# Optimization experiments

Measured on AMD Instinct MI355X. Metric: run time of the kernel, lower is better.

## Reference

```python
import math
import jax, jax.numpy as jnp
import numpy as np

CAPACITY_FACTOR = 1.25
TOP_K = 2
LN_EPS = 1e-5


def setup_inputs() -> dict:
    key = jax.random.key(0)
    ks = jax.random.split(key, 4)
    B, S, D, F, E = 8, 4096, 256, 512, 8
    x = jax.random.normal(ks[0], (B, S, D), dtype=jnp.float32)
    Wr = jax.random.normal(ks[1], (D, E), dtype=jnp.float32) / np.sqrt(D)
    br = jnp.zeros((E,), jnp.float32)
    W1 = jax.random.normal(ks[2], (E, D, F), dtype=jnp.float32) / np.sqrt(D)
    b1 = jnp.zeros((E, F), jnp.float32)
    W2 = jax.random.normal(ks[3], (E, F, D), dtype=jnp.float32) / np.sqrt(F)
    b2 = jnp.zeros((E, D), jnp.float32)
    gamma = jnp.ones((D,), jnp.float32)
    beta = jnp.zeros((D,), jnp.float32)
    return {"x": x, "Wr": Wr, "br": br, "W1": W1, "b1": b1,
            "W2": W2, "b2": b2, "gamma": gamma, "beta": beta}


def _layer_norm(x, gamma, beta):
    mu = jnp.mean(x, axis=-1, keepdims=True)
    var = jnp.var(x, axis=-1, keepdims=True)
    return (x - mu) * jax.lax.rsqrt(var + LN_EPS) * gamma + beta


def reference(x, Wr, br, W1, b1, W2, b2, gamma, beta):
    B, S, D = x.shape
    E = Wr.shape[1]
    N = B * S
    K = TOP_K

    # --- Router: per-sequence softmax routing weights [B, E] ---
    logits = jnp.mean(x, axis=1) @ Wr + br              # [B, E]
    routing_weights = jax.nn.softmax(logits, axis=-1)   # [B, E]

    # --- Capacity constraints (SparseMoELayer._apply_capacity_constraints) ---
    capacity = float(math.ceil(N * CAPACITY_FACTOR / E))
    expected_loads = routing_weights.sum(axis=0) * (N / B)          # [E]
    scale = jnp.where(expected_loads > capacity,
                      capacity / expected_loads, 1.0)               # [E]
    routing_weights = jax.nn.softmax(routing_weights * scale, axis=-1)

    # --- Expand to tokens and take top-k, renormalize with softmax ---
    rw_tok = jnp.broadcast_to(routing_weights[:, None, :], (B, S, E)).reshape(N, E)
    top_w, top_i = jax.lax.top_k(rw_tok, K)             # [N, K]
    top_w = jax.nn.softmax(top_w, axis=-1)

    # --- Expert FFNs (dense compute over all experts, sparse combine) ---
    xf = x.reshape(N, D)
    h = jax.nn.gelu(jnp.einsum('nd,edf->enf', xf, W1) + b1[:, None, :],
                    approximate=False)                  # [E, N, F]
    y = jnp.einsum('enf,efd->end', h, W2) + b2[:, None, :]  # [E, N, D]

    # dense combine weights [N, E] via scatter-add of top-k weights
    w_dense = jnp.zeros((N, E), x.dtype).at[jnp.arange(N)[:, None], top_i].add(top_w)
    out = jnp.einsum('ne,end->nd', w_dense, y).reshape(B, S, D)

    # residual + layer norm
    out = _layer_norm(out + x, gamma, beta)
    return out
```

## Files before the change

kernel.cpp:

```cpp
#include <hip/hip_runtime.h>
#include <math.h>


#define B_ 8
#define S_ 4096
#define D_ 256
#define F_ 512
#define E_ 8

typedef short bf16x8 __attribute__((ext_vector_type(8)));
typedef float f32x4 __attribute__((ext_vector_type(4)));

static __device__ __forceinline__ unsigned short f2bf(float f) {
    union { float f; unsigned int i; } v; v.f = f;
    unsigned int x = v.i;
    return (unsigned short)((x + 0x7fffu + ((x >> 16) & 1u)) >> 16);
}

static __device__ __forceinline__ void bar_lds() {
    asm volatile("s_waitcnt lgkmcnt(0)" ::: "memory");
    __builtin_amdgcn_s_barrier();
}

static __device__ __forceinline__ float gelu_f(float v) {
    float x = fabsf(v) * 0.70710678118654752f;
    float t = __builtin_amdgcn_rcpf(1.0f + 0.3275911f * x);
    float p = t * (0.254829592f +
              t * (-0.284496736f +
              t * (1.421413741f +
              t * (-1.453152027f +
              t * 1.061405429f))));
    float er = 1.0f - p * __expf(-x * x);
    er = __builtin_copysignf(er, v);
    return 0.5f * v * (1.0f + er);
}

__global__ void k_prep(const float* __restrict__ x,
                       double* __restrict__ partial,
                       const float* __restrict__ W1,
                       const float* __restrict__ W2,
                       unsigned short* __restrict__ W1T,
                       unsigned short* __restrict__ W2T) {
    int bid = blockIdx.x;
    if (bid < 512) {
        int b = bid >> 6;
        int c = bid & 63;
        int d = threadIdx.x;
        const float* p = x + ((size_t)(b * S_ + c * 64) * D_ + d);
        double acc = 0.0;
        #pragma unroll 8
        for (int i = 0; i < 64; ++i) acc += (double)p[(size_t)i * D_];
        partial[(size_t)bid * D_ + d] = acc;
        return;
    }
    __shared__ float tile[32][33];
    const float* src;
    unsigned short* dst;
    int R, C, cb, rb;
    if (bid < 1536) {
        int b2 = bid - 512;
        int e = b2 >> 7, rem = b2 & 127;
        int by = rem >> 4, bx = rem & 15;
        R = 256; C = 512;
        src = W1 + (size_t)e * R * C;
        dst = W1T + (size_t)e * R * C;
        cb = bx * 32; rb = by * 32;
    } else {
        int b2 = bid - 1536;
        int e = b2 >> 7, rem = b2 & 127;
        int by = rem >> 3, bx = rem & 7;
        R = 512; C = 256;
        src = W2 + (size_t)e * R * C;
        dst = W2T + (size_t)e * R * C;
        cb = bx * 32; rb = by * 32;
    }
    int tx = threadIdx.x & 31, ty = threadIdx.x >> 5;
    #pragma unroll
    for (int k = 0; k < 4; ++k)
        tile[ty + 8 * k][tx] = src[(size_t)(rb + ty + 8 * k) * C + cb + tx];
    __syncthreads();
    #pragma unroll
    for (int k = 0; k < 4; ++k)
        dst[(size_t)(cb + ty + 8 * k) * R + rb + tx] = f2bf(tile[tx][ty + 8 * k]);
}

__global__ void k_finish(const double* __restrict__ partial,
                         const float* __restrict__ Wr,
                         const float* __restrict__ br,
                         float* __restrict__ route) {
    __shared__ double xs[8][256];
    __shared__ double lg[64];
    __shared__ double rw[8][8];
    int t = threadIdx.x;
    #pragma unroll
    for (int pp = 0; pp < 2; ++pp) {
        int p = pp * 1024 + t;
        int bb = p >> 8, d = p & 255;
        double acc = 0.0;
        #pragma unroll 8
        for (int c = 0; c < 64; ++c)
            acc += partial[(size_t)(bb * 64 + c) * D_ + d];
        xs[bb][d] = acc;
    }
    __syncthreads();
    if (t < 64) {
        int b = t >> 3, e = t & 7;
        double acc = 0.0;
        for (int d = 0; d < D_; ++d)
            acc += (xs[b][d] * (1.0 / (double)S_)) * (double)Wr[d * E_ + e];
        lg[t] = acc + (double)br[e];
    }
    __syncthreads();
    if (t < 8) {
        int bb = t;
        double m = -1e300;
        for (int ee = 0; ee < 8; ++ee) m = fmax(m, lg[bb * 8 + ee]);
        double s = 0.0;
        double p[8];
        for (int ee = 0; ee < 8; ++ee) { p[ee] = exp(lg[bb * 8 + ee] - m); s += p[ee]; }
        for (int ee = 0; ee < 8; ++ee) rw[bb][ee] = p[ee] / s;
    }
    __syncthreads();
    if (t < 8) {
        int bb = t;
        const double capacity = 5120.0;
        double scale[8];
        for (int ee = 0; ee < 8; ++ee) {
            double load = 0.0;
            for (int b2 = 0; b2 < 8; ++b2) load += rw[b2][ee];
            load *= 4096.0;
            scale[ee] = load > capacity ? capacity / load : 1.0;
        }
        double v[8];
        double m = -1e300;
        for (int ee = 0; ee < 8; ++ee) { v[ee] = rw[bb][ee] * scale[ee]; m = fmax(m, v[ee]); }
        double s = 0.0;
        for (int ee = 0; ee < 8; ++ee) { v[ee] = exp(v[ee] - m); s += v[ee]; }
        for (int ee = 0; ee < 8; ++ee) v[ee] /= s;
        int i1 = 0;
        for (int ee = 1; ee < 8; ++ee) if (v[ee] > v[i1]) i1 = ee;
        int i2 = (i1 == 0) ? 1 : 0;
        for (int ee = 0; ee < 8; ++ee) { if (ee == i1) continue; if (v[ee] > v[i2]) i2 = ee; }
        double d21 = v[i2] - v[i1];
        double ed = exp(d21);
        double w1 = 1.0 / (1.0 + ed);
        double w2 = ed * w1;
        route[bb * 4 + 0] = (float)i1;
        route[bb * 4 + 1] = (float)i2;
        route[bb * 4 + 2] = (float)w1;
        route[bb * 4 + 3] = (float)w2;
    }
}

__launch_bounds__(512, 4)
__global__ void k_moe_m(const float* __restrict__ xf,
                        const unsigned short* __restrict__ W1T,
                        const unsigned short* __restrict__ W2T,
                        const float* __restrict__ b1,
                        const float* __restrict__ b2,
                        const float* __restrict__ gamma,
                        const float* __restrict__ beta,
                        const float* __restrict__ route,
                        float* __restrict__ out) {
    __shared__ __align__(16) unsigned short Xsb[64][264];
    __shared__ __align__(16) unsigned short Hsb[2][64][136];
    __shared__ float gbuf[256], bbuf[256];
    __shared__ __align__(16) float rred[64][20];

    const int t = threadIdx.x;
    const int wv = t >> 6;
    const int lane = t & 63;
    const int g = lane >> 4;
    const int c = lane & 15;
    const int b = blockIdx.x & 7;
    const int m0 = (blockIdx.x >> 3) * 64;

    if (t < 256) { gbuf[t] = gamma[t]; bbuf[t] = beta[t]; }

    {
        int row = t >> 3;
        int col0 = (t & 7) * 32;
        const float* src = xf + ((size_t)(b * S_ + m0 + row) * D_ + col0);
        #pragma unroll
        for (int jg = 0; jg < 4; ++jg) {
            float4 a0 = *(const float4*)(src + jg * 8);
            float4 a1 = *(const float4*)(src + jg * 8 + 4);
            float vv[8] = { a0.x, a0.y, a0.z, a0.w, a1.x, a1.y, a1.z, a1.w };
            union { unsigned short u[8]; uint4 q; } o;
            #pragma unroll
            for (int j = 0; j < 8; ++j) o.u[j] = f2bf(vv[j]);
            *(uint4*)&Xsb[row][col0 + jg * 8] = o.q;
        }
    }

    const int e0i = (int)route[b * 4 + 0];
    const int e1i = (int)route[b * 4 + 1];
    const float rw0 = route[b * 4 + 2];
    const float rw1 = route[b * 4 + 3];
    const int eidx[2] = { e0i, e1i };
    const float wgt[2] = { rw0, rw1 };

    f32x4 Yacc[4][2];
    #pragma unroll
    for (int i = 0; i < 4; ++i)
        #pragma unroll
        for (int j = 0; j < 2; ++j)
            #pragma unroll
            for (int r = 0; r < 4; ++r) Yacc[i][j][r] = 0.f;

    bar_lds();

    int pb = 0;
    for (int sl = 0; sl < 2; ++sl) {
        const int e = eidx[sl];
        const float w = wgt[sl];
        for (int fb = 0; fb < 4; ++fb) {
            const unsigned short* w1p =
                W1T + ((size_t)(e * F_ + fb * 128 + wv * 16 + c)) * D_ + g * 8;
            bf16x8 w1f[8];
            #pragma unroll
            for (int kc = 0; kc < 8; ++kc)
                w1f[kc] = *(const bf16x8*)(w1p + kc * 32);
            const unsigned short* w2p =
                W2T + ((size_t)(e * D_ + wv * 32 + c)) * F_ + fb * 128 + g * 8;
            bf16x8 w2f[4][2];
            #pragma unroll
            for (int kc = 0; kc < 4; ++kc)
                #pragma unroll
                for (int nt = 0; nt < 2; ++nt)
                    w2f[kc][nt] = *(const bf16x8*)(w2p + (size_t)(nt * 16) * F_ + kc * 32);
            asm volatile("" : "+v"(w1f[0]), "+v"(w1f[1]), "+v"(w1f[2]), "+v"(w1f[3]),
                              "+v"(w1f[4]), "+v"(w1f[5]), "+v"(w1f[6]), "+v"(w1f[7]));

            f32x4 Hacc[4];
            #pragma unroll
            for (int i = 0; i < 4; ++i)
                #pragma unroll
                for (int r = 0; r < 4; ++r) Hacc[i][r] = 0.f;
            #pragma unroll
            for (int kc = 0; kc < 8; ++kc) {
                #pragma unroll
                for (int mt = 0; mt < 4; ++mt) {
                    bf16x8 a = *(const bf16x8*)&Xsb[mt * 16 + c][kc * 32 + g * 8];
                    Hacc[mt] = __builtin_amdgcn_mfma_f32_16x16x32_bf16(a, w1f[kc], Hacc[mt], 0, 0, 0);
                }
            }

            {
                float bias1 = b1[e * F_ + fb * 128 + wv * 16 + c];
                #pragma unroll
                for (int mt = 0; mt < 4; ++mt)
                    #pragma unroll
                    for (int r = 0; r < 4; ++r) {
                        int row = mt * 16 + g * 4 + r;
                        float v = Hacc[mt][r] + bias1;
                        Hsb[pb][row][wv * 16 + c] = f2bf(w * gelu_f(v));
                    }
            }
            asm volatile("" : "+v"(w2f[0][0]), "+v"(w2f[0][1]), "+v"(w2f[1][0]), "+v"(w2f[1][1]),
                              "+v"(w2f[2][0]), "+v"(w2f[2][1]), "+v"(w2f[3][0]), "+v"(w2f[3][1]));
            bar_lds();

            #pragma unroll
            for (int kc = 0; kc < 4; ++kc) {
                #pragma unroll
                for (int mt = 0; mt < 4; ++mt) {
                    bf16x8 a = *(const bf16x8*)&Hsb[pb][mt * 16 + c][kc * 32 + g * 8];
                    #pragma unroll
                    for (int nt = 0; nt < 2; ++nt)
                        Yacc[mt][nt] = __builtin_amdgcn_mfma_f32_16x16x32_bf16(a, w2f[kc][nt], Yacc[mt][nt], 0, 0, 0);
                }
            }
            pb ^= 1;
        }
    }

    float bias2[2];
    #pragma unroll
    for (int nt = 0; nt < 2; ++nt) {
        int d = wv * 32 + nt * 16 + c;
        bias2[nt] = rw0 * b2[e0i * D_ + d] + rw1 * b2[e1i * D_ + d];
    }
    #pragma unroll
    for (int mt = 0; mt < 4; ++mt)
        #pragma unroll
        for (int r = 0; r < 4; ++r) {
            int row = mt * 16 + g * 4 + r;
            const float* xr = xf + (size_t)(b * S_ + m0 + row) * D_;
            float s = 0.f, sq = 0.f;
            #pragma unroll
            for (int nt = 0; nt < 2; ++nt) {
                int d = wv * 32 + nt * 16 + c;
                float v = Yacc[mt][nt][r] + bias2[nt] + xr[d];
                Yacc[mt][nt][r] = v;
                s += v; sq += v * v;
            }
            s += __shfl_xor(s, 1); sq += __shfl_xor(sq, 1);
            s += __shfl_xor(s, 2); sq += __shfl_xor(sq, 2);
            s += __shfl_xor(s, 4); sq += __shfl_xor(sq, 4);
            s += __shfl_xor(s, 8); sq += __shfl_xor(sq, 8);
            if (c == 0) { rred[row][wv * 2] = s; rred[row][wv * 2 + 1] = sq; }
        }
    bar_lds();
    #pragma unroll
    for (int mt = 0; mt < 4; ++mt)
        #pragma unroll
        for (int r = 0; r < 4; ++r) {
            int row = mt * 16 + g * 4 + r;
            float4 p0 = *(const float4*)&rred[row][0];
            float4 p1 = *(const float4*)&rred[row][4];
            float4 p2 = *(const float4*)&rred[row][8];
            float4 p3 = *(const float4*)&rred[row][12];
            float s  = ((p0.x + p1.x) + (p2.x + p3.x)) + ((p0.z + p1.z) + (p2.z + p3.z));
            float sq = ((p0.y + p1.y) + (p2.y + p3.y)) + ((p0.w + p1.w) + (p2.w + p3.w));
            float mu = s * (1.0f / 256.0f);
            float var = sq * (1.0f / 256.0f) - mu * mu;
            float rstd = rsqrtf(var + 1e-5f);
            float* op = out + (size_t)(b * S_ + m0 + row) * D_;
            #pragma unroll
            for (int nt = 0; nt < 2; ++nt) {
                int d = wv * 32 + nt * 16 + c;
                op[d] = (Yacc[mt][nt][r] - mu) * rstd * gbuf[d] + bbuf[d];
            }
        }
}

extern "C" void kernel_launch(void* const* d_in, const int* in_sizes, int n_in,
                              void* d_out, int out_size, void* d_ws, size_t ws_size,
                              hipStream_t stream) {
    const float* x     = (const float*)d_in[0];
    const float* Wr    = (const float*)d_in[1];
    const float* br    = (const float*)d_in[2];
    const float* W1    = (const float*)d_in[3];
    const float* b1    = (const float*)d_in[4];
    const float* W2    = (const float*)d_in[5];
    const float* b2    = (const float*)d_in[6];
    const float* gamma = (const float*)d_in[7];
    const float* beta  = (const float*)d_in[8];
    float* out = (float*)d_out;

    char* ws = (char*)d_ws;
    double* partial = (double*)ws;
    float* route  = (float*)(ws + 1064960);
    unsigned short* W1T = (unsigned short*)(ws + 1081344);
    unsigned short* W2T = (unsigned short*)(ws + 3178496);

    hipLaunchKernelGGL(k_prep, dim3(2560), dim3(256), 0, stream,
                       x, partial, W1, W2, W1T, W2T);
    hipLaunchKernelGGL(k_finish, dim3(1), dim3(1024), 0, stream,
                       partial, Wr, br, route);
    hipLaunchKernelGGL(k_moe_m, dim3(512), dim3(512), 0, stream,
                       x, W1T, W2T, b1, b2, gamma, beta, route, out);
}
```

Measured before the change: 222.1 us.

## Prefetch next W1 fragment across flattened expert loop and use packed bf16 converts

Flattens the two-level expert/F-block loop into a single eight-iteration loop and issues the W1 fragment loads for the next iteration before the barrier and second GEMM, so global weight latency overlaps with compute. It also replaces the software bf16 rounding with the hardware v_cvt_pk_bf16_f32 instruction for the X staging and the GELU output. The prefetch keeps an extra set of fragment registers live, which may raise register pressure, and the final iteration wastefully reloads the first block.

```diff
diff --git a/kernel.cpp b/kernel.cpp
--- a/kernel.cpp
+++ b/kernel.cpp
@@ -15,6 +15,12 @@
     union { float f; unsigned int i; } v; v.f = f;
     unsigned int x = v.i;
     return (unsigned short)((x + 0x7fffu + ((x >> 16) & 1u)) >> 16);
+}
+
+static __device__ __forceinline__ unsigned int cvt_pk_bf16(float s0, float s1) {
+    unsigned int r;
+    asm("v_cvt_pk_bf16_f32 %0, %1, %2" : "=v"(r) : "v"(s0), "v"(s1));
+    return r;
 }
 
 static __device__ __forceinline__ void bar_lds() {
@@ -177,6 +183,11 @@
 
     if (t < 256) { gbuf[t] = gamma[t]; bbuf[t] = beta[t]; }
 
+    const int e0i = (int)route[b * 4 + 0];
+    const int e1i = (int)route[b * 4 + 1];
+    const float rw0 = route[b * 4 + 2];
+    const float rw1 = route[b * 4 + 3];
+
     {
         int row = t >> 3;
         int col0 = (t & 7) * 32;
@@ -185,21 +196,15 @@
         for (int jg = 0; jg < 4; ++jg) {
             float4 a0 = *(const float4*)(src + jg * 8);
             float4 a1 = *(const float4*)(src + jg * 8 + 4);
-            float vv[8] = { a0.x, a0.y, a0.z, a0.w, a1.x, a1.y, a1.z, a1.w };
-            union { unsigned short u[8]; uint4 q; } o;
-            #pragma unroll
-            for (int j = 0; j < 8; ++j) o.u[j] = f2bf(vv[j]);
+            union { unsigned int pk[4]; uint4 q; } o;
+            o.pk[0] = cvt_pk_bf16(a0.x, a0.y);
+            o.pk[1] = cvt_pk_bf16(a0.z, a0.w);
+            o.pk[2] = cvt_pk_bf16(a1.x, a1.y);
+            o.pk[3] = cvt_pk_bf16(a1.z, a1.w);
             *(uint4*)&Xsb[row][col0 + jg * 8] = o.q;
         }
     }
 
-    const int e0i = (int)route[b * 4 + 0];
-    const int e1i = (int)route[b * 4 + 1];
-    const float rw0 = route[b * 4 + 2];
-    const float rw1 = route[b * 4 + 3];
-    const int eidx[2] = { e0i, e1i };
-    const float wgt[2] = { rw0, rw1 };
-
     f32x4 Yacc[4][2];
     #pragma unroll
     for (int i = 0; i < 4; ++i)
@@ -208,71 +213,91 @@
             #pragma unroll
             for (int r = 0; r < 4; ++r) Yacc[i][j][r] = 0.f;
 
+    bf16x8 w1f[8];
+    {
+        const unsigned short* w1p0 =
+            W1T + ((size_t)(e0i * F_ + wv * 16 + c)) * D_ + g * 8;
+        #pragma unroll
+        for (int kc = 0; kc < 8; ++kc)
+            w1f[kc] = *(const bf16x8*)(w1p0 + kc * 32);
+    }
+
     bar_lds();
 
     int pb = 0;
-    for (int sl = 0; sl < 2; ++sl) {
-        const int e = eidx[sl];
-        const float w = wgt[sl];
-        for (int fb = 0; fb < 4; ++fb) {
-            const unsigned short* w1p =
-                W1T + ((size_t)(e * F_ + fb * 128 + wv * 16 + c)) * D_ + g * 8;
-            bf16x8 w1f[8];
+    for (int it = 0; it < 8; ++it) {
+        const int sl = it >> 2;
+        const int fb = it & 3;
+        const int e = sl ? e1i : e0i;
+        const float w = sl ? rw1 : rw0;
+
+        const unsigned short* w2p =
+            W2T + ((size_t)(e * D_ + wv * 32 + c)) * F_ + fb * 128 + g * 8;
+        bf16x8 w2f[4][2];
+        #pragma unroll
+        for (int kc = 0; kc < 4; ++kc)
+            #pragma unroll
+            for (int nt = 0; nt < 2; ++nt)
+                w2f[kc][nt] = *(const bf16x8*)(w2p + (size_t)(nt * 16) * F_ + kc * 32);
+
+        float bias1 = b1[e * F_ + fb * 128 + wv * 16 + c];
+
+        f32x4 Hacc[4];
+        #pragma unroll
+        for (int i = 0; i < 4; ++i)
+            #pragma unroll
+            for (int r = 0; r < 4; ++r) Hacc[i][r] = 0.f;
+        #pragma unroll
+        for (int kc = 0; kc < 8; ++kc) {
+            #pragma unroll
+            for (int mt = 0; mt < 4; ++mt) {
+                bf16x8 a = *(const bf16x8*)&Xsb[mt * 16 + c][kc * 32 + g * 8];
+                Hacc[mt] = __builtin_amdgcn_mfma_f32_16x16x32_bf16(a, w1f[kc], Hacc[mt], 0, 0, 0);
+            }
+        }
+
+        {
+            const int col = wv * 16 + c;
+            #pragma unroll
+            for (int mt = 0; mt < 4; ++mt) {
+                float h0 = w * gelu_f(Hacc[mt][0] + bias1);
+                float h1 = w * gelu_f(Hacc[mt][1] + bias1);
+                float h2 = w * gelu_f(Hacc[mt][2] + bias1);
+                float h3 = w * gelu_f(Hacc[mt][3] + bias1);
+                unsigned int q01 = cvt_pk_bf16(h0, h1);
+                unsigned int q23 = cvt_pk_bf16(h2, h3);
+                int rowb = mt * 16 + g * 4;
+                Hsb[pb][rowb + 0][col] = (unsigned short)(q01 & 0xffffu);
+                Hsb[pb][rowb + 1][col] = (unsigned short)(q01 >> 16);
+                Hsb[pb][rowb + 2][col] = (unsigned short)(q23 & 0xffffu);
+                Hsb[pb][rowb + 3][col] = (unsigned short)(q23 >> 16);
+            }
+        }
+
+        {
+            const int itn = (it + 1) & 7;
+            const int en = (itn >> 2) ? e1i : e0i;
+            const int fbn = itn & 3;
+            const unsigned short* w1pn =
+                W1T + ((size_t)(en * F_ + fbn * 128 + wv * 16 + c)) * D_ + g * 8;
             #pragma unroll
             for (int kc = 0; kc < 8; ++kc)
-                w1f[kc] = *(const bf16x8*)(w1p + kc * 32);
-            const unsigned short* w2p =
-                W2T + ((size_t)(e * D_ + wv * 32 + c)) * F_ + fb * 128 + g * 8;
-            bf16x8 w2f[4][2];
-            #pragma unroll
-            for (int kc = 0; kc < 4; ++kc)
+                w1f[kc] = *(const bf16x8*)(w1pn + kc * 32);
+        }
+
+        bar_lds();
+
+        #pragma unroll
+        for (int kc = 0; kc < 4; ++kc) {
+            #pragma unroll
+            for (int mt = 0; mt < 4; ++mt) {
+                bf16x8 a = *(const bf16x8*)&Hsb[pb][mt * 16 + c][kc * 32 + g * 8];
                 #pragma unroll
                 for (int nt = 0; nt < 2; ++nt)
-                    w2f[kc][nt] = *(const bf16x8*)(w2p + (size_t)(nt * 16) * F_ + kc * 32);
-            asm volatile("" : "+v"(w1f[0]), "+v"(w1f[1]), "+v"(w1f[2]), "+v"(w1f[3]),
-                              "+v"(w1f[4]), "+v"(w1f[5]), "+v"(w1f[6]), "+v"(w1f[7]));
-
-            f32x4 Hacc[4];
-            #pragma unroll
-            for (int i = 0; i < 4; ++i)
-                #pragma unroll
-                for (int r = 0; r < 4; ++r) Hacc[i][r] = 0.f;
-            #pragma unroll
-            for (int kc = 0; kc < 8; ++kc) {
-                #pragma unroll
-                for (int mt = 0; mt < 4; ++mt) {
-                    bf16x8 a = *(const bf16x8*)&Xsb[mt * 16 + c][kc * 32 + g * 8];
-                    Hacc[mt] = __builtin_amdgcn_mfma_f32_16x16x32_bf16(a, w1f[kc], Hacc[mt], 0, 0, 0);
-                }
-            }
-
-            {
-                float bias1 = b1[e * F_ + fb * 128 + wv * 16 + c];
-                #pragma unroll
-                for (int mt = 0; mt < 4; ++mt)
-                    #pragma unroll
-                    for (int r = 0; r < 4; ++r) {
-                        int row = mt * 16 + g * 4 + r;
-                        float v = Hacc[mt][r] + bias1;
-                        Hsb[pb][row][wv * 16 + c] = f2bf(w * gelu_f(v));
-                    }
-            }
-            asm volatile("" : "+v"(w2f[0][0]), "+v"(w2f[0][1]), "+v"(w2f[1][0]), "+v"(w2f[1][1]),
-                              "+v"(w2f[2][0]), "+v"(w2f[2][1]), "+v"(w2f[3][0]), "+v"(w2f[3][1]));
-            bar_lds();
-
-            #pragma unroll
-            for (int kc = 0; kc < 4; ++kc) {
-                #pragma unroll
-                for (int mt = 0; mt < 4; ++mt) {
-                    bf16x8 a = *(const bf16x8*)&Hsb[pb][mt * 16 + c][kc * 32 + g * 8];
-                    #pragma unroll
-                    for (int nt = 0; nt < 2; ++nt)
-                        Yacc[mt][nt] = __builtin_amdgcn_mfma_f32_16x16x32_bf16(a, w2f[kc][nt], Yacc[mt][nt], 0, 0, 0);
-                }
-            }
-            pb ^= 1;
-        }
+                    Yacc[mt][nt] = __builtin_amdgcn_mfma_f32_16x16x32_bf16(a, w2f[kc][nt], Yacc[mt][nt], 0, 0, 0);
+            }
+        }
+        pb ^= 1;
     }
 
     float bias2[2];
```

After: 213.4 us. -3.9%, faster.
